# Performance work log

Measured on AMD Instinct MI355X. Metric: run time of the kernel, lower is better.

Reference implementation:

```python
import jax, jax.numpy as jnp
import numpy as np

N, D, K, E = 100000, 256, 16, 3200000
COLLAPSE_REG = 0.1


def setup_inputs() -> dict:
    key = jax.random.key(0)
    k1, k2, k3 = jax.random.split(key, 3)
    features = jax.random.normal(k1, (N, D), dtype=jnp.float32)
    edge_index = jax.random.randint(k2, (2, E), 0, N, dtype=jnp.int32)
    adj_vals = jnp.ones((E,), dtype=jnp.float32)
    # orthogonal-ish init for linear weight, zero bias (as in nn.init.orthogonal_/zeros_)
    W = jax.random.normal(k3, (K, D), dtype=jnp.float32) / np.sqrt(D).astype(np.float32)
    b = jnp.zeros((K,), dtype=jnp.float32)
    return {"features": features, "edge_index": edge_index, "adj_vals": adj_vals, "W": W, "b": b}


def reference(features, edge_index, adj_vals, W, b):
    n = features.shape[0]
    k = W.shape[0]
    # cluster assignment: softmax(linear(features)); dropout_rate=0 -> identity
    assignments = jax.nn.softmax(features @ W.T + b, axis=-1)  # [n, k]

    rows, cols = edge_index[0], edge_index[1]
    # node degrees from sparse adjacency (row sums)
    degrees = jax.ops.segment_sum(adj_vals, rows, num_segments=n)  # [n]
    m2 = jnp.sum(degrees)  # 2m (total edge weight * 2)

    # SpMM: (A @ S) via edge-wise gather + segment-sum scatter
    AS = jax.ops.segment_sum(adj_vals[:, None] * assignments[cols], rows, num_segments=n)  # [n, k]
    graph_pooled = assignments.T @ AS  # [k, k] = S^T A S

    # modularity null-model normalizer: (S^T d)(d^T S) / 2m
    left = assignments.T @ degrees  # [k]
    normalizer = jnp.outer(left, left) / m2
    spectral_loss = -jnp.trace(graph_pooled - normalizer) / m2

    cluster_sizes = jnp.sum(assignments, axis=0)  # [k]
    collapse_loss = COLLAPSE_REG * (
        jnp.linalg.norm(cluster_sizes) / n * jnp.sqrt(jnp.float32(k)) - 1.0
    )

    # pooled cluster representations: selu((S / sizes)^T X)  -> [k, d]
    assignments_pooling = assignments / cluster_sizes  # broadcast over clusters
    features_pooled = jax.nn.selu(assignments_pooling.T @ features)
    return features_pooled, assignments, spectral_loss, collapse_loss
```

## Files before the change

### kernel.cpp

```cpp
#include <hip/hip_runtime.h>

#define N_NODES 100000
#define DIM 256
#define KC 16
#define NE 3200000
#define CHUNK 64
#define NCHUNKS ((N_NODES + CHUNK - 1) / CHUNK)

#define D0STR 1168
#define GSTR  144
#define PSTR  72

using bf16x8 = __attribute__((ext_vector_type(8))) short;
using f32x4  = __attribute__((ext_vector_type(4))) float;

__device__ __forceinline__ unsigned short f2bf(float f) {
    unsigned u = __float_as_uint(f);
    return (unsigned short)((u + 0x7fffu + ((u >> 16) & 1u)) >> 16);
}
__device__ __forceinline__ unsigned packbf(float a, float b) {
    return (unsigned)f2bf(a) | ((unsigned)f2bf(b) << 16);
}

template <bool WRITE_PACK>
__global__ __launch_bounds__(256, 4) void k_assign_stx(const float4* __restrict__ X4,
                                                       const float4* __restrict__ W4,
                                                       const float* __restrict__ bias,
                                                       float* __restrict__ S,
                                                       unsigned* __restrict__ Sb,
                                                       float* __restrict__ cs_g,
                                                       float* __restrict__ stx) {
    __shared__ __align__(16) unsigned short Xs[16 * D0STR];
    __shared__ __align__(16) unsigned short psb[16 * PSTR];
    __shared__ float csred[4][KC];

    const int lane = threadIdx.x & 63;
    const int wv   = threadIdx.x >> 6;
    const int c    = lane & 15;
    const int quad = lane >> 4;

    const int base = blockIdx.x * CHUNK;

    const int c4  = threadIdx.x & 63;
    const int r0  = threadIdx.x >> 6;
    const int d0s = c4 >> 2;
    const int wo  = (c4 & 3) * 4;

    float4 xr[8];
    #pragma unroll
    for (int s = 0; s < 8; s++) {
        int rg = base + r0 + 4 * s;
        if (rg >= N_NODES) rg = N_NODES - 1;
        xr[s] = X4[(size_t)rg * 64 + c4];
    }
    bf16x8 wfrag[8];
    #pragma unroll
    for (int s = 0; s < 4; s++) {
        float4 wa = W4[c * 64 + s * 8 + quad * 2];
        float4 wb = W4[c * 64 + s * 8 + quad * 2 + 1];
        union { bf16x8 v; unsigned u[4]; } wf;
        wf.u[0] = packbf(wa.x, wa.y);
        wf.u[1] = packbf(wa.z, wa.w);
        wf.u[2] = packbf(wb.x, wb.y);
        wf.u[3] = packbf(wb.z, wb.w);
        wfrag[s] = wf.v;
    }
    #pragma unroll
    for (int s = 0; s < 8; s++) {
        int r = r0 + 4 * s;
        *(uint2*)&Xs[d0s * D0STR + (r >> 3) * GSTR + (r & 7) * 16 + wo] =
            make_uint2(packbf(xr[s].x, xr[s].y), packbf(xr[s].z, xr[s].w));
    }
    #pragma unroll
    for (int s = 0; s < 8; s++) {
        int rg = base + r0 + 4 * (s + 8);
        if (rg >= N_NODES) rg = N_NODES - 1;
        xr[s] = X4[(size_t)rg * 64 + c4];
    }
    #pragma unroll
    for (int s = 4; s < 8; s++) {
        float4 wa = W4[c * 64 + s * 8 + quad * 2];
        float4 wb = W4[c * 64 + s * 8 + quad * 2 + 1];
        union { bf16x8 v; unsigned u[4]; } wf;
        wf.u[0] = packbf(wa.x, wa.y);
        wf.u[1] = packbf(wa.z, wa.w);
        wf.u[2] = packbf(wb.x, wb.y);
        wf.u[3] = packbf(wb.z, wb.w);
        wfrag[s] = wf.v;
    }
    #pragma unroll
    for (int s = 0; s < 8; s++) {
        int r = r0 + 4 * (s + 8);
        *(uint2*)&Xs[d0s * D0STR + (r >> 3) * GSTR + (r & 7) * 16 + wo] =
            make_uint2(packbf(xr[s].x, xr[s].y), packbf(xr[s].z, xr[s].w));
    }
    const float4 b4 = ((const float4*)bias)[quad];
    __syncthreads();

    f32x4 la = {0.f, 0.f, 0.f, 0.f};
    {
        const int node = wv * 16 + c;
        const int gA = node >> 3, n8 = node & 7;
        #pragma unroll
        for (int s = 0; s < 8; s++) {
            const int d0 = 2 * s + (quad >> 1);
            bf16x8 xf = *(const bf16x8*)&Xs[d0 * D0STR + gA * GSTR + n8 * 16 + (quad & 1) * 8];
            la = __builtin_amdgcn_mfma_f32_16x16x32_bf16(wfrag[s], xf, la, 0, 0, 0);
        }
    }
    float lg0 = la[0] + b4.x, lg1 = la[1] + b4.y;
    float lg2 = la[2] + b4.z, lg3 = la[3] + b4.w;
    float mx = fmaxf(fmaxf(lg0, lg1), fmaxf(lg2, lg3));
    mx = fmaxf(mx, __shfl_xor(mx, 16));
    mx = fmaxf(mx, __shfl_xor(mx, 32));
    float e0 = __expf(lg0 - mx), e1 = __expf(lg1 - mx);
    float e2 = __expf(lg2 - mx), e3 = __expf(lg3 - mx);
    float ssum = e0 + e1 + e2 + e3;
    ssum += __shfl_xor(ssum, 16);
    ssum += __shfl_xor(ssum, 32);
    float inv = 1.f / ssum;
    float pvv[4] = {e0 * inv, e1 * inv, e2 * inv, e3 * inv};

    const int nn = wv * 16 + c;
    const int nd = base + nn;
    if (nd >= N_NODES) {
        pvv[0] = pvv[1] = pvv[2] = pvv[3] = 0.f;
    } else {
        *(float4*)&S[(size_t)nd * KC + quad * 4] =
            make_float4(pvv[0], pvv[1], pvv[2], pvv[3]);
        if (WRITE_PACK) {
            unsigned q0 = __float2uint_rn(pvv[0] * 255.f);
            unsigned q1 = __float2uint_rn(pvv[1] * 255.f);
            unsigned q2 = __float2uint_rn(pvv[2] * 255.f);
            unsigned q3 = __float2uint_rn(pvv[3] * 255.f);
            Sb[(size_t)nd * 4 + quad] = q0 | (q1 << 8) | (q2 << 16) | (q3 << 24);
        }
    }
    float csr[4];
    #pragma unroll
    for (int r = 0; r < 4; r++) {
        psb[(quad * 4 + r) * PSTR + nn] = f2bf(pvv[r]);
        csr[r] = pvv[r];
    }
    __syncthreads();

    f32x4 acc[4];
    #pragma unroll
    for (int t = 0; t < 4; t++) acc[t] = (f32x4){0.f, 0.f, 0.f, 0.f};
    bf16x8 afH[2];
    afH[0] = *(const bf16x8*)&psb[c * PSTR + 0 * 32 + quad * 8];
    afH[1] = *(const bf16x8*)&psb[c * PSTR + 1 * 32 + quad * 8];
    #pragma unroll
    for (int t = 0; t < 4; t++) {
        const int d0  = wv * 4 + t;
        const int dlo = c;
        union { bf16x8 v; unsigned short h[8]; } bf0, bf1;
        #pragma unroll
        for (int j = 0; j < 8; j++) {
            const int n0 = quad * 8 + j;
            bf0.h[j] = Xs[d0 * D0STR + (n0 >> 3) * GSTR + (n0 & 7) * 16 + dlo];
            const int n1 = 32 + n0;
            bf1.h[j] = Xs[d0 * D0STR + (n1 >> 3) * GSTR + (n1 & 7) * 16 + dlo];
        }
        acc[t] = __builtin_amdgcn_mfma_f32_16x16x32_bf16(afH[0], bf0.v, acc[t], 0, 0, 0);
        acc[t] = __builtin_amdgcn_mfma_f32_16x16x32_bf16(afH[1], bf1.v, acc[t], 0, 0, 0);
    }

    #pragma unroll
    for (int t = 0; t < 4; t++) {
        #pragma unroll
        for (int r = 0; r < 4; r++)
            atomicAdd(&stx[(quad * 4 + r) * DIM + (wv * 4 + t) * 16 + c], acc[t][r]);
    }

    #pragma unroll
    for (int r = 0; r < 4; r++) {
        float v = csr[r];
        v += __shfl_xor(v, 1); v += __shfl_xor(v, 2);
        v += __shfl_xor(v, 4); v += __shfl_xor(v, 8);
        csr[r] = v;
    }
    if (c == 0) {
        #pragma unroll
        for (int r = 0; r < 4; r++) csred[wv][quad * 4 + r] = csr[r];
    }
    __syncthreads();
    if (threadIdx.x < KC) {
        int t = threadIdx.x;
        atomicAdd(&cs_g[t], csred[0][t] + csred[1][t] + csred[2][t] + csred[3][t]);
    }
}

__device__ __forceinline__ void edge_acc_u8(uint4 qr, uint4 qc, float a,
                                            float (&lf)[KC], float& m2l, float& trl) {
    union { uint4 v; unsigned w[4]; } R, C;
    R.v = qr; C.v = qc;
    float dd = 0.f;
    #pragma unroll
    for (int q = 0; q < 4; q++) {
        unsigned x = R.w[q], y = C.w[q];
        float s0 = (float)(x & 0xffu);
        float s1 = (float)((x >> 8) & 0xffu);
        float s2 = (float)((x >> 16) & 0xffu);
        float s3 = (float)(x >> 24);
        float c0 = (float)(y & 0xffu);
        float c1 = (float)((y >> 8) & 0xffu);
        float c2 = (float)((y >> 16) & 0xffu);
        float c3 = (float)(y >> 24);
        dd = fmaf(s0, c0, dd); dd = fmaf(s1, c1, dd);
        dd = fmaf(s2, c2, dd); dd = fmaf(s3, c3, dd);
        lf[4 * q + 0] = fmaf(a, s0, lf[4 * q + 0]);
        lf[4 * q + 1] = fmaf(a, s1, lf[4 * q + 1]);
        lf[4 * q + 2] = fmaf(a, s2, lf[4 * q + 2]);
        lf[4 * q + 3] = fmaf(a, s3, lf[4 * q + 3]);
    }
    m2l += a;
    trl = fmaf(a, dd, trl);
}

__global__ __launch_bounds__(256) void k_edges_u8(const int* __restrict__ rows,
                                                  const int* __restrict__ cols,
                                                  const float* __restrict__ adj,
                                                  const uint4* __restrict__ Sb4,
                                                  float* __restrict__ m2_g,
                                                  float* __restrict__ tr_g,
                                                  float* __restrict__ left_g) {
    float m2l = 0.f, trl = 0.f;
    float lf[KC];
    #pragma unroll
    for (int k = 0; k < KC; k++) lf[k] = 0.f;

    const int NU = NE / 4;
    const int stride = gridDim.x * blockDim.x;
    for (int u = blockIdx.x * blockDim.x + threadIdx.x; u < NU; u += stride) {
        int4   r4 = *(const int4*)(rows + 4 * (size_t)u);
        int4   c4 = *(const int4*)(cols + 4 * (size_t)u);
        float4 a4 = *(const float4*)(adj + 4 * (size_t)u);
        uint4 qr0 = Sb4[r4.x];
        uint4 qc0 = Sb4[c4.x];
        uint4 qr1 = Sb4[r4.y];
        uint4 qc1 = Sb4[c4.y];
        uint4 qr2 = Sb4[r4.z];
        uint4 qc2 = Sb4[c4.z];
        uint4 qr3 = Sb4[r4.w];
        uint4 qc3 = Sb4[c4.w];
        edge_acc_u8(qr0, qc0, a4.x, lf, m2l, trl);
        edge_acc_u8(qr1, qc1, a4.y, lf, m2l, trl);
        edge_acc_u8(qr2, qc2, a4.z, lf, m2l, trl);
        edge_acc_u8(qr3, qc3, a4.w, lf, m2l, trl);
    }

    trl *= (1.f / 65025.f);
    #pragma unroll
    for (int k = 0; k < KC; k++) lf[k] *= (1.f / 255.f);

    #pragma unroll
    for (int off = 32; off >= 1; off >>= 1) {
        m2l += __shfl_xor(m2l, off);
        trl += __shfl_xor(trl, off);
    }
    #pragma unroll
    for (int k = 0; k < KC; k++) {
        float v = lf[k];
        #pragma unroll
        for (int off = 32; off >= 1; off >>= 1) v += __shfl_xor(v, off);
        lf[k] = v;
    }
    __shared__ float red[4][18];
    int w = threadIdx.x >> 6;
    if ((threadIdx.x & 63) == 0) {
        red[w][0] = m2l; red[w][1] = trl;
        #pragma unroll
        for (int k = 0; k < KC; k++) red[w][2 + k] = lf[k];
    }
    __syncthreads();
    int t = threadIdx.x;
    if (t < 18) {
        float v = red[0][t] + red[1][t] + red[2][t] + red[3][t];
        float* dst = (t == 0) ? m2_g : (t == 1) ? tr_g : &left_g[t - 2];
        atomicAdd(dst, v);
    }
}

__global__ __launch_bounds__(256) void k_edges_f32(const int* __restrict__ rows,
                                                   const int* __restrict__ cols,
                                                   const float* __restrict__ adj,
                                                   const float* __restrict__ S,
                                                   float* __restrict__ m2_g,
                                                   float* __restrict__ tr_g,
                                                   float* __restrict__ left_g) {
    float m2l = 0.f, trl = 0.f;
    float lf[KC];
    #pragma unroll
    for (int k = 0; k < KC; k++) lf[k] = 0.f;

    int stride = gridDim.x * blockDim.x;
    for (int e = blockIdx.x * blockDim.x + threadIdx.x; e < NE; e += stride) {
        int r = rows[e], c = cols[e];
        float a = adj[e];
        float sv[KC], cv[KC];
        const float4* sr = (const float4*)(S + (size_t)r * KC);
        const float4* sc = (const float4*)(S + (size_t)c * KC);
        #pragma unroll
        for (int qq = 0; qq < 4; qq++) {
            float4 s4 = sr[qq], c4 = sc[qq];
            sv[4*qq]=s4.x; sv[4*qq+1]=s4.y; sv[4*qq+2]=s4.z; sv[4*qq+3]=s4.w;
            cv[4*qq]=c4.x; cv[4*qq+1]=c4.y; cv[4*qq+2]=c4.z; cv[4*qq+3]=c4.w;
        }
        float dd = 0.f;
        #pragma unroll
        for (int k = 0; k < KC; k++) {
            dd += sv[k] * cv[k];
            lf[k] += a * sv[k];
        }
        m2l += a;
        trl += a * dd;
    }

    #pragma unroll
    for (int off = 32; off >= 1; off >>= 1) {
        m2l += __shfl_xor(m2l, off);
        trl += __shfl_xor(trl, off);
    }
    #pragma unroll
    for (int k = 0; k < KC; k++) {
        float v = lf[k];
        #pragma unroll
        for (int off = 32; off >= 1; off >>= 1) v += __shfl_xor(v, off);
        lf[k] = v;
    }
    __shared__ float red[4][18];
    int w = threadIdx.x >> 6;
    if ((threadIdx.x & 63) == 0) {
        red[w][0] = m2l; red[w][1] = trl;
        #pragma unroll
        for (int k = 0; k < KC; k++) red[w][2 + k] = lf[k];
    }
    __syncthreads();
    int t = threadIdx.x;
    if (t < 18) {
        float v = red[0][t] + red[1][t] + red[2][t] + red[3][t];
        float* dst = (t == 0) ? m2_g : (t == 1) ? tr_g : &left_g[t - 2];
        atomicAdd(dst, v);
    }
}

__global__ __launch_bounds__(256) void k_final(const float* __restrict__ cs,
                                               const float* __restrict__ left,
                                               const float* __restrict__ m2p,
                                               const float* __restrict__ trp,
                                               const float* __restrict__ stx,
                                               float* __restrict__ out) {
    int t = threadIdx.x;
    #pragma unroll
    for (int k = 0; k < KC; k++) {
        float v = stx[k * DIM + t] / cs[k];
        float r = (v > 0.f) ? 1.0507009873554805f * v
                            : 1.7580993408473766f * (__expf(v) - 1.f);
        out[k * DIM + t] = r;
    }
    if (t == 0) {
        float m2 = *m2p;
        float tn = 0.f;
        #pragma unroll
        for (int k = 0; k < KC; k++) tn += left[k] * left[k];
        tn /= m2;
        float spectral = -((*trp) - tn) / m2;
        float ss = 0.f;
        #pragma unroll
        for (int k = 0; k < KC; k++) ss += cs[k] * cs[k];
        float collapse = 0.1f * (sqrtf(ss) / (float)N_NODES * 4.0f - 1.0f);
        out[KC * DIM + (size_t)N_NODES * KC]     = spectral;
        out[KC * DIM + (size_t)N_NODES * KC + 1] = collapse;
    }
}

extern "C" void kernel_launch(void* const* d_in, const int* in_sizes, int n_in,
                              void* d_out, int out_size, void* d_ws, size_t ws_size,
                              hipStream_t stream) {
    (void)out_size;

    const float* X    = nullptr;
    const int*   ei   = nullptr;
    const float* adj  = nullptr;
    const float* W    = nullptr;
    const float* bias = nullptr;
    for (int i = 0; i < n_in; i++) {
        switch (in_sizes[i]) {
            case 25600000: X    = (const float*)d_in[i]; break;
            case  6400000: ei   = (const int*)d_in[i];   break;
            case  3200000: adj  = (const float*)d_in[i]; break;
            case     4096: W    = (const float*)d_in[i]; break;
            case       16: bias = (const float*)d_in[i]; break;
        }
    }

    float* out = (float*)d_out;
    float* S   = out + KC * DIM;
    const int* rows = ei;
    const int* cols = ei + NE;

    float* ws   = (float*)d_ws;
    float* cs   = ws;
    float* left = ws + 16;
    float* m2   = ws + 32;
    float* tr   = ws + 33;
    float* stx  = ws + 64;
    unsigned* Sb = (unsigned*)(ws + 64 + KC * DIM);
    const size_t need = (64 + KC * DIM) * sizeof(float) + (size_t)N_NODES * 16;
    const bool use_pack = (ws_size >= need);

    hipMemsetAsync(d_ws, 0, (64 + KC * DIM) * sizeof(float), stream);

    if (use_pack) {
        k_assign_stx<true><<<NCHUNKS, 256, 0, stream>>>(
            (const float4*)X, (const float4*)W, bias, S, Sb, cs, stx);
        k_edges_u8<<<2048, 256, 0, stream>>>(rows, cols, adj, (const uint4*)Sb,
                                             m2, tr, left);
    } else {
        k_assign_stx<false><<<NCHUNKS, 256, 0, stream>>>(
            (const float4*)X, (const float4*)W, bias, S, Sb, cs, stx);
        k_edges_f32<<<2048, 256, 0, stream>>>(rows, cols, adj, S, m2, tr, left);
    }
    k_final<<<1, 256, 0, stream>>>(cs, left, m2, tr, stx, out);
}
```

Measured before the change: 248.0 us.

## Replace S^T X atomics with per-block partials and a separate reduce kernel

Each assignment block now writes its 16x256 S^T X partial tile to a workspace buffer with plain vector stores, replacing per-element global atomics. A new reduce kernel sums the partials across all chunks and applies the cluster-size normalization and SELU, and a small kernel computes the losses. The edge kernel also processes two edges per iteration instead of four, giving more iterations with fewer outstanding gathers each. The partials path adds about 6.4 MB of workspace traffic and two extra launches, and it only runs when the workspace is large enough.

```diff
diff --git a/kernel.cpp b/kernel.cpp
--- a/kernel.cpp
+++ b/kernel.cpp
@@ -22,14 +22,15 @@
     return (unsigned)f2bf(a) | ((unsigned)f2bf(b) << 16);
 }
 
-template <bool WRITE_PACK>
+template <bool WRITE_PACK, bool WRITE_PART>
 __global__ __launch_bounds__(256, 4) void k_assign_stx(const float4* __restrict__ X4,
                                                        const float4* __restrict__ W4,
                                                        const float* __restrict__ bias,
                                                        float* __restrict__ S,
                                                        unsigned* __restrict__ Sb,
                                                        float* __restrict__ cs_g,
-                                                       float* __restrict__ stx) {
+                                                       float* __restrict__ stx,
+                                                       float* __restrict__ Pb) {
     __shared__ __align__(16) unsigned short Xs[16 * D0STR];
     __shared__ __align__(16) unsigned short psb[16 * PSTR];
     __shared__ float csred[4][KC];
@@ -166,28 +167,81 @@
         acc[t] = __builtin_amdgcn_mfma_f32_16x16x32_bf16(afH[1], bf1.v, acc[t], 0, 0, 0);
     }
 
-    #pragma unroll
-    for (int t = 0; t < 4; t++) {
-        #pragma unroll
-        for (int r = 0; r < 4; r++)
-            atomicAdd(&stx[(quad * 4 + r) * DIM + (wv * 4 + t) * 16 + c], acc[t][r]);
-    }
-
+    if (WRITE_PART) {
+        #pragma unroll
+        for (int t = 0; t < 4; t++) {
+            *(float4*)&Pb[((size_t)blockIdx.x * 256 + (wv * 4 + t) * 16 + c) * 16 + quad * 4] =
+                make_float4(acc[t][0], acc[t][1], acc[t][2], acc[t][3]);
+        }
+    } else {
+        #pragma unroll
+        for (int t = 0; t < 4; t++) {
+            #pragma unroll
+            for (int r = 0; r < 4; r++)
+                atomicAdd(&stx[(quad * 4 + r) * DIM + (wv * 4 + t) * 16 + c], acc[t][r]);
+        }
+    }
+
+    float csr2[4];
     #pragma unroll
     for (int r = 0; r < 4; r++) {
         float v = csr[r];
         v += __shfl_xor(v, 1); v += __shfl_xor(v, 2);
         v += __shfl_xor(v, 4); v += __shfl_xor(v, 8);
-        csr[r] = v;
+        csr2[r] = v;
     }
     if (c == 0) {
         #pragma unroll
-        for (int r = 0; r < 4; r++) csred[wv][quad * 4 + r] = csr[r];
+        for (int r = 0; r < 4; r++) csred[wv][quad * 4 + r] = csr2[r];
     }
     __syncthreads();
     if (threadIdx.x < KC) {
         int t = threadIdx.x;
         atomicAdd(&cs_g[t], csred[0][t] + csred[1][t] + csred[2][t] + csred[3][t]);
+    }
+}
+
+__global__ __launch_bounds__(256) void k_reduce(const float* __restrict__ Pb,
+                                                const float* __restrict__ cs,
+                                                float* __restrict__ out) {
+    const int d  = blockIdx.x;
+    const int k  = threadIdx.x & 15;
+    const int bg = threadIdx.x >> 4;
+    float s = 0.f;
+    for (int b = bg; b < NCHUNKS; b += 16)
+        s += Pb[((size_t)b * 256 + d) * 16 + k];
+    __shared__ float red[16][17];
+    red[bg][k] = s;
+    __syncthreads();
+    if (threadIdx.x < 16) {
+        float v = 0.f;
+        #pragma unroll
+        for (int g = 0; g < 16; g++) v += red[g][threadIdx.x];
+        float q = v / cs[threadIdx.x];
+        float r = (q > 0.f) ? 1.0507009873554805f * q
+                            : 1.7580993408473766f * (__expf(q) - 1.f);
+        out[threadIdx.x * DIM + d] = r;
+    }
+}
+
+__global__ void k_losses(const float* __restrict__ cs,
+                         const float* __restrict__ left,
+                         const float* __restrict__ m2p,
+                         const float* __restrict__ trp,
+                         float* __restrict__ out) {
+    if (threadIdx.x == 0) {
+        float m2 = *m2p;
+        float tn = 0.f;
+        #pragma unroll
+        for (int k = 0; k < KC; k++) tn += left[k] * left[k];
+        tn /= m2;
+        float spectral = -((*trp) - tn) / m2;
+        float ss = 0.f;
+        #pragma unroll
+        for (int k = 0; k < KC; k++) ss += cs[k] * cs[k];
+        float collapse = 0.1f * (sqrtf(ss) / (float)N_NODES * 4.0f - 1.0f);
+        out[KC * DIM + (size_t)N_NODES * KC]     = spectral;
+        out[KC * DIM + (size_t)N_NODES * KC + 1] = collapse;
     }
 }
 
@@ -230,24 +284,18 @@
     #pragma unroll
     for (int k = 0; k < KC; k++) lf[k] = 0.f;
 
-    const int NU = NE / 4;
+    const int NU = NE / 2;
     const int stride = gridDim.x * blockDim.x;
     for (int u = blockIdx.x * blockDim.x + threadIdx.x; u < NU; u += stride) {
-        int4   r4 = *(const int4*)(rows + 4 * (size_t)u);
-        int4   c4 = *(const int4*)(cols + 4 * (size_t)u);
-        float4 a4 = *(const float4*)(adj + 4 * (size_t)u);
-        uint4 qr0 = Sb4[r4.x];
-        uint4 qc0 = Sb4[c4.x];
-        uint4 qr1 = Sb4[r4.y];
-        uint4 qc1 = Sb4[c4.y];
-        uint4 qr2 = Sb4[r4.z];
-        uint4 qc2 = Sb4[c4.z];
-        uint4 qr3 = Sb4[r4.w];
-        uint4 qc3 = Sb4[c4.w];
-        edge_acc_u8(qr0, qc0, a4.x, lf, m2l, trl);
-        edge_acc_u8(qr1, qc1, a4.y, lf, m2l, trl);
-        edge_acc_u8(qr2, qc2, a4.z, lf, m2l, trl);
-        edge_acc_u8(qr3, qc3, a4.w, lf, m2l, trl);
+        int2   r2 = *(const int2*)(rows + 2 * (size_t)u);
+        int2   c2 = *(const int2*)(cols + 2 * (size_t)u);
+        float2 a2 = *(const float2*)(adj + 2 * (size_t)u);
+        uint4 qr0 = Sb4[r2.x];
+        uint4 qc0 = Sb4[c2.x];
+        uint4 qr1 = Sb4[r2.y];
+        uint4 qc1 = Sb4[c2.y];
+        edge_acc_u8(qr0, qc0, a2.x, lf, m2l, trl);
+        edge_acc_u8(qr1, qc1, a2.y, lf, m2l, trl);
     }
 
     trl *= (1.f / 65025.f);
@@ -407,20 +455,31 @@
     float* tr   = ws + 33;
     float* stx  = ws + 64;
     unsigned* Sb = (unsigned*)(ws + 64 + KC * DIM);
-    const size_t need = (64 + KC * DIM) * sizeof(float) + (size_t)N_NODES * 16;
-    const bool use_pack = (ws_size >= need);
+    float* Pb    = (float*)(Sb + (size_t)N_NODES * 4);
+    const size_t need_pack = (64 + KC * DIM) * sizeof(float) + (size_t)N_NODES * 16;
+    const size_t need_part = need_pack + (size_t)NCHUNKS * 4096 * sizeof(float);
+    const bool use_pack = (ws_size >= need_pack);
+    const bool use_part = (ws_size >= need_part);
 
     hipMemsetAsync(d_ws, 0, (64 + KC * DIM) * sizeof(float), stream);
 
-    if (use_pack) {
-        k_assign_stx<true><<<NCHUNKS, 256, 0, stream>>>(
-            (const float4*)X, (const float4*)W, bias, S, Sb, cs, stx);
+    if (use_part) {
+        k_assign_stx<true, true><<<NCHUNKS, 256, 0, stream>>>(
+            (const float4*)X, (const float4*)W, bias, S, Sb, cs, stx, Pb);
         k_edges_u8<<<2048, 256, 0, stream>>>(rows, cols, adj, (const uint4*)Sb,
                                              m2, tr, left);
+        k_reduce<<<DIM, 256, 0, stream>>>(Pb, cs, out);
+        k_losses<<<1, 64, 0, stream>>>(cs, left, m2, tr, out);
+    } else if (use_pack) {
+        k_assign_stx<true, false><<<NCHUNKS, 256, 0, stream>>>(
+            (const float4*)X, (const float4*)W, bias, S, Sb, cs, stx, nullptr);
+        k_edges_u8<<<2048, 256, 0, stream>>>(rows, cols, adj, (const uint4*)Sb,
+                                             m2, tr, left);
+        k_final<<<1, 256, 0, stream>>>(cs, left, m2, tr, stx, out);
     } else {
-        k_assign_stx<false><<<NCHUNKS, 256, 0, stream>>>(
-            (const float4*)X, (const float4*)W, bias, S, Sb, cs, stx);
+        k_assign_stx<false, false><<<NCHUNKS, 256, 0, stream>>>(
+            (const float4*)X, (const float4*)W, bias, S, Sb, cs, stx, nullptr);
         k_edges_f32<<<2048, 256, 0, stream>>>(rows, cols, adj, S, m2, tr, left);
-    }
-    k_final<<<1, 256, 0, stream>>>(cs, left, m2, tr, stx, out);
-}
+        k_final<<<1, 256, 0, stream>>>(cs, left, m2, tr, stx, out);
+    }
+}
```

After: 254.5 us. 2.6% more time.
